# Kernel optimization log

Hardware: AMD Instinct MI355X
Metric: run time of the kernel (lower is better)

## Reference

```python
import jax, jax.numpy as jnp
import numpy as np

DYNAMIC_RANGE = 16  # from init_kwargs
MAX_VAL = 2 ** (DYNAMIC_RANGE - 1) - 1   # 32767
MIN_VAL = -(2 ** (DYNAMIC_RANGE - 1))    # -32768


def setup_inputs() -> dict:
    key = jax.random.key(0)
    k_img, k_w = jax.random.split(key)
    Z, Y, X = 128, 512, 512
    P = 15                      # prediction_bands
    image = jax.random.normal(k_img, (Z, Y, X), dtype=jnp.float32) * 100.0
    # weights buffer is [num_bands, 4 + prediction_bands]; original inits to zeros
    # (degenerate output), so we use small random weights in [-1, 1].
    weights = jax.random.normal(k_w, (Z, 4 + P), dtype=jnp.float32) * 0.05
    return {"image": image, "weights": weights}


def reference(image, weights):
    # image: [Z, Y, X], weights: [Z, 4 + P]
    Z, Y, X = image.shape
    P = weights.shape[1] - 4

    # Note: sample_representatives[z] = predictions[z] + residuals[z] = image[z],
    # so all neighbor extraction operates on the raw image. Weight updates in the
    # original only touch weights[z] AFTER band z is predicted and that row is
    # never read again, so the output depends only on the initial weights.

    # Spatial neighbors (zero-padded): N, W, NW, (N+W+NW)/3  -> [Z, Y, X, 4]
    pad = jnp.pad(image, ((0, 0), (1, 1), (1, 1)))
    north = pad[:, :-2, 1:-1]
    west = pad[:, 1:-1, :-2]
    northwest = pad[:, :-2, :-2]
    fourth = (north + west + northwest) / 3
    spatial = jnp.stack([north, west, northwest, fourth], axis=-1)

    # Spectral neighbors: bands z-P .. z-1, zero-padded at the front.
    # spec_pad[z + p] == image[z - P + p] (or 0 if out of range) -> [P, Z, Y, X]
    spec_pad = jnp.concatenate(
        [jnp.zeros((P, Y, X), dtype=image.dtype), image], axis=0)
    spectral = jnp.stack([spec_pad[p:p + Z] for p in range(P)], axis=0)

    # Per-band weighted sum over the 4 + P predictors, then clamp.
    pred = (jnp.einsum('zyxs,zs->zyx', spatial, weights[:, :4])
            + jnp.einsum('pzyx,zp->zyx', spectral, weights[:, 4:]))
    pred = jnp.clip(pred, MIN_VAL, MAX_VAL)

    residuals = image - pred
    return pred, residuals
```

## Files before the change

### kernel.cpp

```cpp
#include <hip/hip_runtime.h>

#define Zdim 128
#define Ydim 512
#define Xdim 512
#define Pdim 15
#define NWt  19
#define CHUNK 32

typedef __attribute__((ext_vector_type(4))) float f4;
struct F4 { float v[4]; };

__device__ __forceinline__ F4 ld4(const float* p) {
    f4 t = *(const f4*)p;
    F4 r; r.v[0] = t[0]; r.v[1] = t[1]; r.v[2] = t[2]; r.v[3] = t[3];
    return r;
}

__global__ __launch_bounds__(256, 4) void spec_pred_kernel(
    const float* __restrict__ img,
    const float* __restrict__ wts,
    float* __restrict__ out)
{
    __shared__ float sw[Zdim * NWt];
    for (int i = threadIdx.x; i < Zdim * NWt; i += 256) sw[i] = wts[i];
    __syncthreads();

    const int bid = blockIdx.x;
    const int zc  = bid >> 8;
    const int id  = ((bid & 255) << 8) | threadIdx.x;
    const int xg  = (id & 127) << 2;
    const int y   = id >> 7;

    const size_t plane = (size_t)Ydim * Xdim;
    const size_t pix   = (size_t)y * Xdim + xg;
    const float* ip = img + pix;
    float* pp = out + pix;
    float* rp = out + (size_t)Zdim * plane + pix;

    const int  z0 = zc * CHUNK;
    const bool hn = (y > 0);
    const bool hw = (xg > 0);

    F4 h[Pdim];
    if (z0 == 0) {
#pragma unroll
        for (int p = 0; p < Pdim; ++p) h[p] = F4{{0, 0, 0, 0}};
    } else {
#pragma unroll
        for (int p = 0; p < Pdim; ++p)
            h[p] = ld4(ip + (size_t)(z0 - Pdim + p) * plane);
    }

    F4 c0, n0, c1, n1;
    float we0, nw0, we1, nw1;

    auto LOAD = [&](int z, F4& c, F4& n, float& we, float& nw) {
        const float* p0 = ip + (size_t)z * plane;
        c  = ld4(p0);
        n  = hn ? ld4(p0 - Xdim) : F4{{0, 0, 0, 0}};
        we = hw ? p0[-1] : 0.0f;
        nw = (hn && hw) ? p0[-Xdim - 1] : 0.0f;
    };

    auto STEP = [&](int z, const F4& c, const F4& n, float we, float nw) {
        const float* wz = &sw[z * NWt];
        const float w3 = wz[3] * (1.0f / 3.0f);
        const float a0 = wz[0] + w3, a1 = wz[1] + w3, a2 = wz[2] + w3;
        f4 pv, rv;
#pragma unroll
        for (int e = 0; e < 4; ++e) {
            const float vn = n.v[e];
            const float vw = e ? c.v[e - 1] : we;
            const float vq = e ? n.v[e - 1] : nw;
            float a = a0 * vn;
            a = fmaf(a1, vw, a);
            a = fmaf(a2, vq, a);
#pragma unroll
            for (int p = 0; p < Pdim; ++p) a = fmaf(wz[4 + p], h[p].v[e], a);
            a = fminf(fmaxf(a, -32768.0f), 32767.0f);
            pv[e] = a;
            rv[e] = c.v[e] - a;
        }
        __builtin_nontemporal_store(pv, (f4*)(pp + (size_t)z * plane));
        __builtin_nontemporal_store(rv, (f4*)(rp + (size_t)z * plane));
#pragma unroll
        for (int p = 0; p < Pdim - 1; ++p) h[p] = h[p + 1];
        h[Pdim - 1] = c;
    };

    LOAD(z0, c0, n0, we0, nw0);
    for (int i = 0; i < CHUNK; i += 2) {
        const int z = z0 + i;
        LOAD(z + 1, c1, n1, we1, nw1);
        STEP(z, c0, n0, we0, nw0);
        if (i + 2 < CHUNK) LOAD(z + 2, c0, n0, we0, nw0);
        STEP(z + 1, c1, n1, we1, nw1);
    }
}

extern "C" void kernel_launch(void* const* d_in, const int* in_sizes, int n_in,
                              void* d_out, int out_size, void* d_ws, size_t ws_size,
                              hipStream_t stream) {
    const float* img = (const float*)d_in[0];
    const float* wts = (const float*)d_in[1];
    float* out = (float*)d_out;

    const int grid = 256 * (Zdim / CHUNK);
    spec_pred_kernel<<<grid, 256, 0, stream>>>(img, wts, out);
}
```

Baseline: 83.73 us.

## Drop shared-memory weight staging and deepen load prefetch to a three-slot ring

```diff
diff --git a/kernel.cpp b/kernel.cpp
--- a/kernel.cpp
+++ b/kernel.cpp
@@ -21,10 +21,6 @@
     const float* __restrict__ wts,
     float* __restrict__ out)
 {
-    __shared__ float sw[Zdim * NWt];
-    for (int i = threadIdx.x; i < Zdim * NWt; i += 256) sw[i] = wts[i];
-    __syncthreads();
-
     const int bid = blockIdx.x;
     const int zc  = bid >> 8;
     const int id  = ((bid & 255) << 8) | threadIdx.x;
@@ -51,27 +47,27 @@
             h[p] = ld4(ip + (size_t)(z0 - Pdim + p) * plane);
     }
 
-    F4 c0, n0, c1, n1;
-    float we0, nw0, we1, nw1;
+    F4 cb[3], nb[3];
+    float wb[3], qb[3];
 
-    auto LOAD = [&](int z, F4& c, F4& n, float& we, float& nw) {
+    auto LOAD = [&](int z, int b) {
         const float* p0 = ip + (size_t)z * plane;
-        c  = ld4(p0);
-        n  = hn ? ld4(p0 - Xdim) : F4{{0, 0, 0, 0}};
-        we = hw ? p0[-1] : 0.0f;
-        nw = (hn && hw) ? p0[-Xdim - 1] : 0.0f;
+        cb[b] = ld4(p0);
+        nb[b] = hn ? ld4(p0 - Xdim) : F4{{0, 0, 0, 0}};
+        wb[b] = hw ? p0[-1] : 0.0f;
+        qb[b] = (hn && hw) ? p0[-Xdim - 1] : 0.0f;
     };
 
-    auto STEP = [&](int z, const F4& c, const F4& n, float we, float nw) {
-        const float* wz = &sw[z * NWt];
+    auto STEP = [&](int z, int b) {
+        const float* wz = wts + z * NWt;
         const float w3 = wz[3] * (1.0f / 3.0f);
         const float a0 = wz[0] + w3, a1 = wz[1] + w3, a2 = wz[2] + w3;
         f4 pv, rv;
 #pragma unroll
         for (int e = 0; e < 4; ++e) {
-            const float vn = n.v[e];
-            const float vw = e ? c.v[e - 1] : we;
-            const float vq = e ? n.v[e - 1] : nw;
+            const float vn = nb[b].v[e];
+            const float vw = e ? cb[b].v[e - 1] : wb[b];
+            const float vq = e ? nb[b].v[e - 1] : qb[b];
             float a = a0 * vn;
             a = fmaf(a1, vw, a);
             a = fmaf(a2, vq, a);
@@ -79,23 +75,24 @@
             for (int p = 0; p < Pdim; ++p) a = fmaf(wz[4 + p], h[p].v[e], a);
             a = fminf(fmaxf(a, -32768.0f), 32767.0f);
             pv[e] = a;
-            rv[e] = c.v[e] - a;
+            rv[e] = cb[b].v[e] - a;
         }
         __builtin_nontemporal_store(pv, (f4*)(pp + (size_t)z * plane));
         __builtin_nontemporal_store(rv, (f4*)(rp + (size_t)z * plane));
 #pragma unroll
         for (int p = 0; p < Pdim - 1; ++p) h[p] = h[p + 1];
-        h[Pdim - 1] = c;
+        h[Pdim - 1] = cb[b];
     };
 
-    LOAD(z0, c0, n0, we0, nw0);
-    for (int i = 0; i < CHUNK; i += 2) {
-        const int z = z0 + i;
-        LOAD(z + 1, c1, n1, we1, nw1);
-        STEP(z, c0, n0, we0, nw0);
-        if (i + 2 < CHUNK) LOAD(z + 2, c0, n0, we0, nw0);
-        STEP(z + 1, c1, n1, we1, nw1);
+    LOAD(z0 + 0, 0);
+    LOAD(z0 + 1, 1);
+#pragma unroll 6
+    for (int i = 0; i < CHUNK - 2; ++i) {
+        LOAD(z0 + i + 2, (i + 2) % 3);
+        STEP(z0 + i, i % 3);
     }
+    STEP(z0 + CHUNK - 2, (CHUNK - 2) % 3);
+    STEP(z0 + CHUNK - 1, (CHUNK - 1) % 3);
 }
 
 extern "C" void kernel_launch(void* const* d_in, const int* in_sizes, int n_in,
```

New measurement: 79.42 us. 1.05x faster.
